# Kernel optimization log

Measured on AMD Instinct MI355X. Metric: run time of the kernel, lower is better.

## Reference

```python
import jax, jax.numpy as jnp
import numpy as np

N_EMBD = 1024
VOCAB = 64
B, T = 8, 4096


def setup_inputs() -> dict:
    key = jax.random.key(0)
    ks = jax.random.split(key, 6)
    x = jax.random.normal(ks[0], (B, T, N_EMBD), dtype=jnp.float32)
    idx = jax.random.randint(ks[1], (B, T), 0, VOCAB, dtype=jnp.int64)
    emb_weight = jax.random.normal(ks[2], (VOCAB, N_EMBD), dtype=jnp.float32)
    head_weight = jax.random.normal(ks[3], (VOCAB, N_EMBD), dtype=jnp.float32)
    gate = jax.random.normal(ks[4], (1, 1, N_EMBD), dtype=jnp.float32) * 0.01
    soft_gate = jax.random.normal(ks[5], (1, 1, N_EMBD), dtype=jnp.float32) * 0.01
    return {"x": x, "idx": idx, "emb_weight": emb_weight,
            "head_weight": head_weight, "gate": gate, "soft_gate": soft_gate}


def reference(x, idx, emb_weight, head_weight, gate, soft_gate):
    # --- idx-gated codebook blend (idx from previous step's argmax, clamped >= 0) ---
    idx_c = jnp.clip(idx, 0, None)
    emb = emb_weight[idx_c]                                  # [B,T,D]
    g = jax.nn.sigmoid(x * gate).mean(axis=-1, keepdims=True)  # [B,T,1]
    x = x * (1.0 - g) + emb * g
    # (tmix/cmix are external and treated as identity here)
    # --- small-vocab head + softmax-weighted codebook lookup ---
    logits = jnp.einsum('btd,vd->btv', x, head_weight)        # [B,T,64]
    soft_prob = jax.nn.softmax(logits, axis=-1)
    soft_emb = jnp.einsum('btv,vd->btd', soft_prob, emb_weight)
    sg = jax.nn.sigmoid(x * soft_gate).mean(axis=-1, keepdims=True)
    x = x * (1.0 - sg) + soft_emb * sg
    # --- argmax indexing for next step ---
    new_idx = jnp.argmax(logits, axis=-1)                     # [B,T]
    return x, new_idx
```

## Files before the change

### kernel.cpp

```cpp
#include <hip/hip_runtime.h>
#include <hip/hip_bf16.h>


#define DIMS 1024
#define VOCAB 64
#define NTOK 32768
#define TTILE 16
#define TPB 256
#define IDX_OFF (NTOK * DIMS)

typedef __attribute__((ext_vector_type(8))) short short8;
typedef __attribute__((ext_vector_type(4))) float f32x4;

__device__ __forceinline__ float sigm(float z) {
    return 1.f / (1.f + __expf(-z));
}
__device__ __forceinline__ unsigned short f2bf(float f) {
    __hip_bfloat16 h = __float2bfloat16(f);
    return *reinterpret_cast<unsigned short*>(&h);
}

__global__ void prep_weights(const float* __restrict__ head,
                             const float* __restrict__ emb,
                             __hip_bfloat16* __restrict__ headB,
                             __hip_bfloat16* __restrict__ embT) {
    int t = blockIdx.x * 256 + threadIdx.x;
    int v = t >> 10, d = t & 1023;
    headB[t] = __float2bfloat16(head[t]);
    embT[d * VOCAB + v] = __float2bfloat16(emb[v * DIMS + d]);
}

__global__ __launch_bounds__(TPB, 2) void fused_block(
    const float* __restrict__ x,
    const int* __restrict__ idx,
    const float* __restrict__ emb,
    const float* __restrict__ gate,
    const float* __restrict__ sgate,
    const float* __restrict__ headF,
    const __hip_bfloat16* __restrict__ headB,
    const __hip_bfloat16* __restrict__ embT,
    float* __restrict__ out)
{
    __shared__ __align__(16) __hip_bfloat16 sX1b[TTILE][1032];
    __shared__ __align__(16) float          sLog[TTILE][68];
    __shared__ __align__(16) __hip_bfloat16 sP[TTILE][72];
    __shared__ float sSg[TTILE];
    __shared__ int   sCand[TTILE][4];

    const int tid  = threadIdx.x;
    const int tk   = tid >> 4;
    const int l16i = tid & 15;
    const long t0  = (long)blockIdx.x * TTILE;
    const long tok = t0 + tk;

    float4 xv[16];
    float gsum = 0.f;
    const float4* xrow = (const float4*)(x + tok * DIMS);
    const float4* grow = (const float4*)gate;
    #pragma unroll
    for (int c = 0; c < 16; c++) {
        int f = l16i + c * 16;
        float4 v = xrow[f];
        float4 gv = grow[f];
        xv[c] = v;
        gsum += sigm(v.x * gv.x) + sigm(v.y * gv.y)
              + sigm(v.z * gv.z) + sigm(v.w * gv.w);
    }
    gsum += __shfl_xor(gsum, 1); gsum += __shfl_xor(gsum, 2);
    gsum += __shfl_xor(gsum, 4); gsum += __shfl_xor(gsum, 8);
    const float g = gsum * (1.f / 1024.f);

    int ic = idx[tok]; if (ic < 0) ic = 0;
    const float4* erow = (const float4*)(emb + (long)ic * DIMS);
    const float4* srow = (const float4*)sgate;
    float ssum = 0.f;
    #pragma unroll
    for (int c = 0; c < 16; c++) {
        int f = l16i + c * 16;
        float4 ev = erow[f];
        float4 sv = srow[f];
        float4 a;
        a.x = xv[c].x * (1.f - g) + ev.x * g;
        a.y = xv[c].y * (1.f - g) + ev.y * g;
        a.z = xv[c].z * (1.f - g) + ev.z * g;
        a.w = xv[c].w * (1.f - g) + ev.w * g;
        xv[c] = a;
        ssum += sigm(a.x * sv.x) + sigm(a.y * sv.y)
              + sigm(a.z * sv.z) + sigm(a.w * sv.w);
        ushort4 pk;
        pk.x = f2bf(a.x); pk.y = f2bf(a.y); pk.z = f2bf(a.z); pk.w = f2bf(a.w);
        *(ushort4*)&sX1b[tk][f * 4] = pk;
    }
    ssum += __shfl_xor(ssum, 1); ssum += __shfl_xor(ssum, 2);
    ssum += __shfl_xor(ssum, 4); ssum += __shfl_xor(ssum, 8);
    if (l16i == 0) sSg[tk] = ssum * (1.f / 1024.f);
    __syncthreads();

    const int w    = tid >> 6;
    const int lane = tid & 63;
    const int quad = lane >> 4, l16 = lane & 15;
    {
        f32x4 acc = {0.f, 0.f, 0.f, 0.f};
        const __hip_bfloat16* hrow = headB + (long)(w * 16 + l16) * DIMS + quad * 8;
        #pragma unroll 4
        for (int k0 = 0; k0 < DIMS; k0 += 32) {
            short8 a = *(const short8*)&sX1b[l16][k0 + quad * 8];
            short8 b = *(const short8*)(hrow + k0);
            acc = __builtin_amdgcn_mfma_f32_16x16x32_bf16(a, b, acc, 0, 0, 0);
        }
        #pragma unroll
        for (int i = 0; i < 4; i++)
            sLog[quad * 4 + i][w * 16 + l16] = acc[i];
    }
    __syncthreads();

    #pragma unroll
    for (int it = 0; it < 4; it++) {
        int m = it * 4 + w;
        float l0 = sLog[m][lane];
        float mx = l0;
        mx = fmaxf(mx, __shfl_xor(mx, 1));  mx = fmaxf(mx, __shfl_xor(mx, 2));
        mx = fmaxf(mx, __shfl_xor(mx, 4));  mx = fmaxf(mx, __shfl_xor(mx, 8));
        mx = fmaxf(mx, __shfl_xor(mx, 16)); mx = fmaxf(mx, __shfl_xor(mx, 32));
        float e = __expf(l0 - mx);
        float s = e;
        s += __shfl_xor(s, 1);  s += __shfl_xor(s, 2);  s += __shfl_xor(s, 4);
        s += __shfl_xor(s, 8);  s += __shfl_xor(s, 16); s += __shfl_xor(s, 32);
        sP[m][lane] = __float2bfloat16(e / s);
        float l = l0;
        int c0i, c1i, c2i, c3i;
        {
            float mj = l;
            mj = fmaxf(mj, __shfl_xor(mj, 1));  mj = fmaxf(mj, __shfl_xor(mj, 2));
            mj = fmaxf(mj, __shfl_xor(mj, 4));  mj = fmaxf(mj, __shfl_xor(mj, 8));
            mj = fmaxf(mj, __shfl_xor(mj, 16)); mj = fmaxf(mj, __shfl_xor(mj, 32));
            c0i = __ffsll(__ballot(l == mj)) - 1; if (lane == c0i) l = -3.4e38f;
        }
        {
            float mj = l;
            mj = fmaxf(mj, __shfl_xor(mj, 1));  mj = fmaxf(mj, __shfl_xor(mj, 2));
            mj = fmaxf(mj, __shfl_xor(mj, 4));  mj = fmaxf(mj, __shfl_xor(mj, 8));
            mj = fmaxf(mj, __shfl_xor(mj, 16)); mj = fmaxf(mj, __shfl_xor(mj, 32));
            c1i = __ffsll(__ballot(l == mj)) - 1; if (lane == c1i) l = -3.4e38f;
        }
        {
            float mj = l;
            mj = fmaxf(mj, __shfl_xor(mj, 1));  mj = fmaxf(mj, __shfl_xor(mj, 2));
            mj = fmaxf(mj, __shfl_xor(mj, 4));  mj = fmaxf(mj, __shfl_xor(mj, 8));
            mj = fmaxf(mj, __shfl_xor(mj, 16)); mj = fmaxf(mj, __shfl_xor(mj, 32));
            c2i = __ffsll(__ballot(l == mj)) - 1; if (lane == c2i) l = -3.4e38f;
        }
        {
            float mj = l;
            mj = fmaxf(mj, __shfl_xor(mj, 1));  mj = fmaxf(mj, __shfl_xor(mj, 2));
            mj = fmaxf(mj, __shfl_xor(mj, 4));  mj = fmaxf(mj, __shfl_xor(mj, 8));
            mj = fmaxf(mj, __shfl_xor(mj, 16)); mj = fmaxf(mj, __shfl_xor(mj, 32));
            c3i = __ffsll(__ballot(l == mj)) - 1;
        }
        if (lane == 0) {
            sCand[m][0] = c0i; sCand[m][1] = c1i;
            sCand[m][2] = c2i; sCand[m][3] = c3i;
        }
    }
    __syncthreads();

    {
        int rows[4];
        #pragma unroll
        for (int j = 0; j < 4; j++) rows[j] = sCand[tk][j];
        float tot[4];
        #pragma unroll
        for (int j = 0; j < 4; j++) {
            const float4* hr = (const float4*)(headF + (long)rows[j] * DIMS);
            float p = 0.f;
            #pragma unroll
            for (int c = 0; c < 16; c++) {
                float4 h = hr[l16i + c * 16];
                p = fmaf(xv[c].x, h.x, p); p = fmaf(xv[c].y, h.y, p);
                p = fmaf(xv[c].z, h.z, p); p = fmaf(xv[c].w, h.w, p);
            }
            p += __shfl_xor(p, 1); p += __shfl_xor(p, 2);
            p += __shfl_xor(p, 4); p += __shfl_xor(p, 8);
            tot[j] = p;
        }
        if (l16i == 0) {
            float bv = tot[0]; int bi = rows[0];
            #pragma unroll
            for (int j = 1; j < 4; j++) {
                if (tot[j] > bv || (tot[j] == bv && rows[j] < bi)) {
                    bv = tot[j]; bi = rows[j];
                }
            }
            out[IDX_OFF + tok] = (float)bi;
        }
    }

    #pragma unroll 1
    for (int i = 0; i < 16; i++) {
        int n0 = (i * 4 + w) * 16;
        f32x4 acc = {0.f, 0.f, 0.f, 0.f};
        #pragma unroll
        for (int k0 = 0; k0 < VOCAB; k0 += 32) {
            short8 a = *(const short8*)&sP[l16][k0 + quad * 8];
            short8 b = *(const short8*)(embT + (long)(n0 + l16) * VOCAB + k0 + quad * 8);
            acc = __builtin_amdgcn_mfma_f32_16x16x32_bf16(a, b, acc, 0, 0, 0);
        }
        #pragma unroll
        for (int r = 0; r < 4; r++) {
            int m = quad * 4 + r;
            int n = n0 + l16;
            float sg = sSg[m];
            float x1f = __bfloat162float(sX1b[m][n]);
            out[(t0 + m) * (long)DIMS + n] = x1f * (1.f - sg) + acc[r] * sg;
        }
    }
}

extern "C" void kernel_launch(void* const* d_in, const int* in_sizes, int n_in,
                              void* d_out, int out_size, void* d_ws, size_t ws_size,
                              hipStream_t stream) {
    const float* xp    = (const float*)d_in[0];
    const int*   idxp  = (const int*)d_in[1];
    const float* embp  = (const float*)d_in[2];
    const float* headp = (const float*)d_in[3];
    const float* gp    = (const float*)d_in[4];
    const float* sgp   = (const float*)d_in[5];
    float*       outp  = (float*)d_out;

    __hip_bfloat16* headB = (__hip_bfloat16*)d_ws;
    __hip_bfloat16* embT  = (__hip_bfloat16*)((char*)d_ws + 131072);

    prep_weights<<<dim3(256), dim3(256), 0, stream>>>(headp, embp, headB, embT);
    fused_block<<<dim3(NTOK / TTILE), dim3(TPB), 0, stream>>>(
        xp, idxp, embp, gp, sgp, headp, headB, embT, outp);
}
```

Before: 313.4 us.

## Double threads per block, split head GEMM over K, keep candidates in registers

Raises the block size from 256 to 512 threads, with 32 threads per token instead of 16, and sets launch bounds to 6 blocks per CU. The head logit MFMA is split into two K halves across 8 waves, and the partial sums are added during the softmax pass. Top-4 argmax candidates stay in registers because each wave's two tokens map onto its two 32-lane halves, which removes the sCand shared array and one barrier. The aim is more parallelism and latency hiding per tile, at the cost of register pressure under the tighter launch bound and an extra reduction step.

New measurement: 309.1 us. Within noise of the previous version (-1.4%).

```diff
diff --git a/kernel.cpp b/kernel.cpp
--- a/kernel.cpp
+++ b/kernel.cpp
@@ -6,7 +6,7 @@
 #define VOCAB 64
 #define NTOK 32768
 #define TTILE 16
-#define TPB 256
+#define TPB 512
 #define IDX_OFF (NTOK * DIMS)
 
 typedef __attribute__((ext_vector_type(8))) short short8;
@@ -30,7 +30,7 @@
     embT[d * VOCAB + v] = __float2bfloat16(emb[v * DIMS + d]);
 }
 
-__global__ __launch_bounds__(TPB, 2) void fused_block(
+__global__ __launch_bounds__(TPB, 6) void fused_block(
     const float* __restrict__ x,
     const int* __restrict__ idx,
     const float* __restrict__ emb,
@@ -42,24 +42,23 @@
     float* __restrict__ out)
 {
     __shared__ __align__(16) __hip_bfloat16 sX1b[TTILE][1032];
-    __shared__ __align__(16) float          sLog[TTILE][68];
+    __shared__ __align__(16) float          sLogP[2][TTILE][68];
     __shared__ __align__(16) __hip_bfloat16 sP[TTILE][72];
     __shared__ float sSg[TTILE];
-    __shared__ int   sCand[TTILE][4];
 
     const int tid  = threadIdx.x;
-    const int tk   = tid >> 4;
-    const int l16i = tid & 15;
+    const int tk   = tid >> 5;
+    const int l32  = tid & 31;
     const long t0  = (long)blockIdx.x * TTILE;
     const long tok = t0 + tk;
 
-    float4 xv[16];
+    float4 xv[8];
     float gsum = 0.f;
     const float4* xrow = (const float4*)(x + tok * DIMS);
     const float4* grow = (const float4*)gate;
     #pragma unroll
-    for (int c = 0; c < 16; c++) {
-        int f = l16i + c * 16;
+    for (int c = 0; c < 8; c++) {
+        int f = l32 + c * 32;
         float4 v = xrow[f];
         float4 gv = grow[f];
         xv[c] = v;
@@ -68,6 +67,7 @@
     }
     gsum += __shfl_xor(gsum, 1); gsum += __shfl_xor(gsum, 2);
     gsum += __shfl_xor(gsum, 4); gsum += __shfl_xor(gsum, 8);
+    gsum += __shfl_xor(gsum, 16);
     const float g = gsum * (1.f / 1024.f);
 
     int ic = idx[tok]; if (ic < 0) ic = 0;
@@ -75,8 +75,8 @@
     const float4* srow = (const float4*)sgate;
     float ssum = 0.f;
     #pragma unroll
-    for (int c = 0; c < 16; c++) {
-        int f = l16i + c * 16;
+    for (int c = 0; c < 8; c++) {
+        int f = l32 + c * 32;
         float4 ev = erow[f];
         float4 sv = srow[f];
         float4 a;
@@ -93,31 +93,35 @@
     }
     ssum += __shfl_xor(ssum, 1); ssum += __shfl_xor(ssum, 2);
     ssum += __shfl_xor(ssum, 4); ssum += __shfl_xor(ssum, 8);
-    if (l16i == 0) sSg[tk] = ssum * (1.f / 1024.f);
+    ssum += __shfl_xor(ssum, 16);
+    if (l32 == 0) sSg[tk] = ssum * (1.f / 1024.f);
     __syncthreads();
 
     const int w    = tid >> 6;
     const int lane = tid & 63;
     const int quad = lane >> 4, l16 = lane & 15;
+    const int nt   = w & 3;
+    const int kh   = w >> 2;
     {
         f32x4 acc = {0.f, 0.f, 0.f, 0.f};
-        const __hip_bfloat16* hrow = headB + (long)(w * 16 + l16) * DIMS + quad * 8;
+        const __hip_bfloat16* hrow = headB + (long)(nt * 16 + l16) * DIMS + kh * 512 + quad * 8;
         #pragma unroll 4
-        for (int k0 = 0; k0 < DIMS; k0 += 32) {
-            short8 a = *(const short8*)&sX1b[l16][k0 + quad * 8];
+        for (int k0 = 0; k0 < 512; k0 += 32) {
+            short8 a = *(const short8*)&sX1b[l16][kh * 512 + k0 + quad * 8];
             short8 b = *(const short8*)(hrow + k0);
             acc = __builtin_amdgcn_mfma_f32_16x16x32_bf16(a, b, acc, 0, 0, 0);
         }
         #pragma unroll
         for (int i = 0; i < 4; i++)
-            sLog[quad * 4 + i][w * 16 + l16] = acc[i];
+            sLogP[kh][quad * 4 + i][nt * 16 + l16] = acc[i];
     }
     __syncthreads();
 
+    int cA[4], cB[4];
     #pragma unroll
-    for (int it = 0; it < 4; it++) {
-        int m = it * 4 + w;
-        float l0 = sLog[m][lane];
+    for (int it = 0; it < 2; it++) {
+        int m = 2 * w + it;
+        float l0 = sLogP[0][m][lane] + sLogP[1][m][lane];
         float mx = l0;
         mx = fmaxf(mx, __shfl_xor(mx, 1));  mx = fmaxf(mx, __shfl_xor(mx, 2));
         mx = fmaxf(mx, __shfl_xor(mx, 4));  mx = fmaxf(mx, __shfl_xor(mx, 8));
@@ -128,62 +132,40 @@
         s += __shfl_xor(s, 8);  s += __shfl_xor(s, 16); s += __shfl_xor(s, 32);
         sP[m][lane] = __float2bfloat16(e / s);
         float l = l0;
-        int c0i, c1i, c2i, c3i;
-        {
+        #pragma unroll
+        for (int j = 0; j < 4; j++) {
             float mj = l;
             mj = fmaxf(mj, __shfl_xor(mj, 1));  mj = fmaxf(mj, __shfl_xor(mj, 2));
             mj = fmaxf(mj, __shfl_xor(mj, 4));  mj = fmaxf(mj, __shfl_xor(mj, 8));
             mj = fmaxf(mj, __shfl_xor(mj, 16)); mj = fmaxf(mj, __shfl_xor(mj, 32));
-            c0i = __ffsll(__ballot(l == mj)) - 1; if (lane == c0i) l = -3.4e38f;
-        }
-        {
-            float mj = l;
-            mj = fmaxf(mj, __shfl_xor(mj, 1));  mj = fmaxf(mj, __shfl_xor(mj, 2));
-            mj = fmaxf(mj, __shfl_xor(mj, 4));  mj = fmaxf(mj, __shfl_xor(mj, 8));
-            mj = fmaxf(mj, __shfl_xor(mj, 16)); mj = fmaxf(mj, __shfl_xor(mj, 32));
-            c1i = __ffsll(__ballot(l == mj)) - 1; if (lane == c1i) l = -3.4e38f;
-        }
-        {
-            float mj = l;
-            mj = fmaxf(mj, __shfl_xor(mj, 1));  mj = fmaxf(mj, __shfl_xor(mj, 2));
-            mj = fmaxf(mj, __shfl_xor(mj, 4));  mj = fmaxf(mj, __shfl_xor(mj, 8));
-            mj = fmaxf(mj, __shfl_xor(mj, 16)); mj = fmaxf(mj, __shfl_xor(mj, 32));
-            c2i = __ffsll(__ballot(l == mj)) - 1; if (lane == c2i) l = -3.4e38f;
-        }
-        {
-            float mj = l;
-            mj = fmaxf(mj, __shfl_xor(mj, 1));  mj = fmaxf(mj, __shfl_xor(mj, 2));
-            mj = fmaxf(mj, __shfl_xor(mj, 4));  mj = fmaxf(mj, __shfl_xor(mj, 8));
-            mj = fmaxf(mj, __shfl_xor(mj, 16)); mj = fmaxf(mj, __shfl_xor(mj, 32));
-            c3i = __ffsll(__ballot(l == mj)) - 1;
-        }
-        if (lane == 0) {
-            sCand[m][0] = c0i; sCand[m][1] = c1i;
-            sCand[m][2] = c2i; sCand[m][3] = c3i;
-        }
-    }
-    __syncthreads();
+            int cj = __ffsll(__ballot(l == mj)) - 1;
+            if (lane == cj) l = -3.4e38f;
+            if (it == 0) cA[j] = cj; else cB[j] = cj;
+        }
+    }
 
     {
+        const int h = (lane >> 5) & 1;
         int rows[4];
         #pragma unroll
-        for (int j = 0; j < 4; j++) rows[j] = sCand[tk][j];
+        for (int j = 0; j < 4; j++) rows[j] = h ? cB[j] : cA[j];
         float tot[4];
         #pragma unroll
         for (int j = 0; j < 4; j++) {
             const float4* hr = (const float4*)(headF + (long)rows[j] * DIMS);
             float p = 0.f;
             #pragma unroll
-            for (int c = 0; c < 16; c++) {
-                float4 h = hr[l16i + c * 16];
-                p = fmaf(xv[c].x, h.x, p); p = fmaf(xv[c].y, h.y, p);
-                p = fmaf(xv[c].z, h.z, p); p = fmaf(xv[c].w, h.w, p);
+            for (int c = 0; c < 8; c++) {
+                float4 hv = hr[l32 + c * 32];
+                p = fmaf(xv[c].x, hv.x, p); p = fmaf(xv[c].y, hv.y, p);
+                p = fmaf(xv[c].z, hv.z, p); p = fmaf(xv[c].w, hv.w, p);
             }
             p += __shfl_xor(p, 1); p += __shfl_xor(p, 2);
             p += __shfl_xor(p, 4); p += __shfl_xor(p, 8);
+            p += __shfl_xor(p, 16);
             tot[j] = p;
         }
-        if (l16i == 0) {
+        if (l32 == 0) {
             float bv = tot[0]; int bi = rows[0];
             #pragma unroll
             for (int j = 1; j < 4; j++) {
@@ -194,10 +176,11 @@
             out[IDX_OFF + tok] = (float)bi;
         }
     }
+    __syncthreads();
 
     #pragma unroll 1
-    for (int i = 0; i < 16; i++) {
-        int n0 = (i * 4 + w) * 16;
+    for (int i = 0; i < 8; i++) {
+        int n0 = (i * 8 + w) * 16;
         f32x4 acc = {0.f, 0.f, 0.f, 0.f};
         #pragma unroll
         for (int k0 = 0; k0 < VOCAB; k0 += 32) {
```
